# Performance work log

Measured on AMD Instinct MI355X. Metric: run time of the kernel, lower is better.

The kernel has to match this reference:

```python
import jax, jax.numpy as jnp
import numpy as np

N_LINKS = 10000
N_PATHS = 50000
PLEN = 5                 # fixed path length -> max_len
E = N_PATHS * PLEN       # number of (link, path) edge entries
D = 32                   # link_state_dim == path_state_dim
H = 32
RU = 256                 # readout_units
T_ITERS = 8              # message-passing iterations t


def setup_inputs() -> dict:
    key = jax.random.key(0)
    ks = jax.random.split(key, 20)
    s = 0.1
    inp = {}
    inp["traffic"] = jax.random.uniform(ks[0], (N_PATHS,), dtype=jnp.float32)
    inp["packets"] = jax.random.uniform(ks[1], (N_PATHS,), dtype=jnp.float32)
    inp["time_dist_params"] = jax.random.normal(ks[2], (N_PATHS, 12), dtype=jnp.float32)
    inp["capacity"] = jax.random.uniform(ks[3], (N_LINKS,), dtype=jnp.float32)
    # edge lists: each path has exactly PLEN links
    inp["link_to_path"] = jax.random.randint(ks[4], (E,), 0, N_LINKS, dtype=jnp.int32)
    inp["path_ids"] = jnp.repeat(jnp.arange(N_PATHS, dtype=jnp.int32), PLEN)
    inp["sequence_path"] = jnp.tile(jnp.arange(PLEN, dtype=jnp.int32), N_PATHS)
    inp["path_to_link"] = jax.random.randint(ks[5], (E,), 0, N_PATHS, dtype=jnp.int32)
    inp["sequence_links"] = jax.random.randint(ks[6], (E,), 0, N_LINKS, dtype=jnp.int32)
    inp["n_links"] = N_LINKS
    inp["n_paths"] = N_PATHS
    # path-update GRU (input D -> hidden H), torch layout [3H, in]
    inp["Wi_p"] = jax.random.normal(ks[7], (3 * H, D), dtype=jnp.float32) * s
    inp["Wh_p"] = jax.random.normal(ks[8], (3 * H, H), dtype=jnp.float32) * s
    inp["bi_p"] = jnp.zeros((3 * H,), jnp.float32)
    inp["bh_p"] = jnp.zeros((3 * H,), jnp.float32)
    # link-update GRUCell (input H -> hidden D)
    inp["Wi_l"] = jax.random.normal(ks[9], (3 * D, H), dtype=jnp.float32) * s
    inp["Wh_l"] = jax.random.normal(ks[10], (3 * D, D), dtype=jnp.float32) * s
    inp["bi_l"] = jnp.zeros((3 * D,), jnp.float32)
    inp["bh_l"] = jnp.zeros((3 * D,), jnp.float32)
    # readout MLP
    inp["W1"] = jax.random.normal(ks[11], (RU, H), dtype=jnp.float32) * s
    inp["b1"] = jnp.zeros((RU,), jnp.float32)
    inp["W2"] = jax.random.normal(ks[12], (RU, RU), dtype=jnp.float32) * s
    inp["b2"] = jnp.zeros((RU,), jnp.float32)
    inp["W3"] = jax.random.normal(ks[13], (1, RU), dtype=jnp.float32) * s
    inp["b3"] = jnp.zeros((1,), jnp.float32)
    return inp


def _gru_step(x, h, Wi, Wh, bi, bh):
    # torch GRU gate math
    gi = x @ Wi.T + bi
    gh = h @ Wh.T + bh
    ir, iz, in_ = jnp.split(gi, 3, axis=-1)
    hr, hz, hn = jnp.split(gh, 3, axis=-1)
    r = jax.nn.sigmoid(ir + hr)
    z = jax.nn.sigmoid(iz + hz)
    n = jnp.tanh(in_ + r * hn)
    return (1.0 - z) * n + z * h


def reference(traffic, packets, time_dist_params, capacity,
              link_to_path, path_ids, sequence_path, path_to_link, sequence_links,
              n_links, n_paths,
              Wi_p, Wh_p, bi_p, bh_p, Wi_l, Wh_l, bi_l, bh_l,
              W1, b1, W2, b2, W3, b3):
    max_len = PLEN  # == sequence_path.max() + 1 (static)
    # per-path valid lengths (equivalent to the torch nonzero-row count loop)
    lens = jax.ops.segment_max(sequence_path, path_ids, num_segments=n_paths) + 1
    link_state = jnp.concatenate(
        [capacity[:, None], jnp.zeros((n_links, D - 1), capacity.dtype)], axis=1)
    path_state = jnp.concatenate(
        [traffic[:, None], packets[:, None], time_dist_params,
         jnp.zeros((n_paths, D - 14), traffic.dtype)], axis=1)

    for _ in range(T_ITERS):
        link_gather = link_state[link_to_path]  # [E, D]
        link_inputs = jnp.zeros((n_paths, max_len, D), link_state.dtype)
        link_inputs = link_inputs.at[path_ids, sequence_path].set(link_gather)

        def step(h, xt_t):
            xt, t = xt_t
            h_new = _gru_step(xt, h, Wi_p, Wh_p, bi_p, bh_p)
            h = jnp.where((t < lens)[:, None], h_new, h)  # pack_padded semantics
            return h, None

        path_state, _ = jax.lax.scan(
            step, path_state,
            (jnp.swapaxes(link_inputs, 0, 1), jnp.arange(max_len)))

        path_gather = path_state[path_to_link]  # [E, H]
        path_sum = jnp.zeros((n_links, H), path_gather.dtype).at[sequence_links].add(path_gather)
        link_state = _gru_step(path_sum, link_state, Wi_l, Wh_l, bi_l, bh_l)

    r = jax.nn.relu(path_state @ W1.T + b1)
    r = jax.nn.relu(r @ W2.T + b2)
    r = r @ W3.T + b3            # [n_paths, 1]
    return r[:, 0][None, :]      # [1, n_paths]
```

## Files before the change

kernel.cpp:

```cpp
#include <hip/hip_runtime.h>

#define NP 50000
#define NL 10000
#define PLEN 5
#define NE (NP * PLEN)
#define DD 32
#define RUU 256
#define TITERS 8
#define PPW 8
#define LPW 2

__device__ __forceinline__ float sigmoidf_(float a) {
    return 1.0f / (1.0f + __expf(-a));
}
__device__ __forceinline__ float tanhf_(float a) {
    a = fminf(fmaxf(a, -15.0f), 15.0f);
    float t = __expf(2.0f * a);
    return (t - 1.0f) / (t + 1.0f);
}

__global__ __launch_bounds__(256) void k_init(
    const float* __restrict__ traffic, const float* __restrict__ packets,
    const float* __restrict__ tdp, const float* __restrict__ capacity,
    float* __restrict__ path_state, float* __restrict__ link_state,
    int* __restrict__ lens, int* __restrict__ cnt) {
    int i = blockIdx.x * 256 + threadIdx.x;
    if (i < NP) {
        float v[DD];
        v[0] = traffic[i];
        v[1] = packets[i];
#pragma unroll
        for (int k = 0; k < 12; k++) v[2 + k] = tdp[i * 12 + k];
#pragma unroll
        for (int k = 14; k < DD; k++) v[k] = 0.0f;
#pragma unroll
        for (int k = 0; k < DD; k++) path_state[i * DD + k] = v[k];
        lens[i] = 0;
    }
    if (i < NL) {
        link_state[i * DD] = capacity[i];
#pragma unroll
        for (int k = 1; k < DD; k++) link_state[i * DD + k] = 0.0f;
        cnt[i] = 0;
    }
}

__global__ __launch_bounds__(256) void k_lens(const int* __restrict__ path_ids,
                                              const int* __restrict__ seq_path,
                                              int* __restrict__ lens) {
    int e = blockIdx.x * 256 + threadIdx.x;
    if (e < NE) atomicMax(&lens[path_ids[e]], seq_path[e] + 1);
}

__global__ __launch_bounds__(256) void k_csr_count(const int* __restrict__ seq_links,
                                                   int* __restrict__ cnt) {
    int e = blockIdx.x * 256 + threadIdx.x;
    if (e < NE) atomicAdd(&cnt[seq_links[e]], 1);
}

__global__ __launch_bounds__(256) void k_csr_scan(const int* __restrict__ cnt,
                                                  int* __restrict__ offs,
                                                  int* __restrict__ cursor) {
    __shared__ int ssum[256];
    const int tid = threadIdx.x;
    const int CH = 40;
    int base = tid * CH;
    int s = 0;
    for (int i = 0; i < CH; i++) {
        int idx = base + i;
        s += (idx < NL) ? cnt[idx] : 0;
    }
    ssum[tid] = s;
    __syncthreads();
    for (int off = 1; off < 256; off <<= 1) {
        int t = (tid >= off) ? ssum[tid - off] : 0;
        __syncthreads();
        ssum[tid] += t;
        __syncthreads();
    }
    int run = ssum[tid] - s;
    for (int i = 0; i < CH; i++) {
        int idx = base + i;
        if (idx < NL) {
            offs[idx] = run;
            cursor[idx] = run;
            run += cnt[idx];
        }
    }
    if (tid == 0) offs[NL] = ssum[255];
}

__global__ __launch_bounds__(256) void k_csr_fill(const int* __restrict__ seq_links,
                                                  const int* __restrict__ path_to_link,
                                                  int* __restrict__ cursor,
                                                  int* __restrict__ csr_pids) {
    int e = blockIdx.x * 256 + threadIdx.x;
    if (e < NE) {
        int l = seq_links[e];
        int slot = atomicAdd(&cursor[l], 1);
        csr_pids[slot] = path_to_link[e];
    }
}

__global__ __launch_bounds__(256) void k_w2t(const float* __restrict__ W2,
                                             float* __restrict__ W2t) {
    int j = blockIdx.x, k = threadIdx.x;
    W2t[k * RUU + j] = W2[j * RUU + k];
}

__global__ __launch_bounds__(256, 2) void k_gru_paths(
    const float* __restrict__ link_state, float* __restrict__ path_state,
    const int* __restrict__ link_to_path, const int* __restrict__ lens,
    const float* __restrict__ Wi, const float* __restrict__ Wh,
    const float* __restrict__ bi, const float* __restrict__ bh) {
    const int tid = threadIdx.x;
    const int wave = tid >> 6;
    const int lane = tid & 63;
    const int d = lane & 31;
    const int half = lane >> 5;

    float wi[3][16], wh[3][16];
#pragma unroll
    for (int g = 0; g < 3; g++) {
        const float* wip = &Wi[(g * 32 + d) * 32 + half * 16];
        const float* whp = &Wh[(g * 32 + d) * 32 + half * 16];
#pragma unroll
        for (int c = 0; c < 4; c++) {
            *(float4*)&wi[g][c * 4] = *(const float4*)&wip[c * 4];
            *(float4*)&wh[g][c * 4] = *(const float4*)&whp[c * 4];
        }
    }
#pragma unroll
    for (int g = 0; g < 3; g++)
#pragma unroll
        for (int k = 0; k < 16; k++) {
            asm volatile("" : "+v"(wi[g][k]));
            asm volatile("" : "+v"(wh[g][k]));
        }
    const float bir = bi[d], biz = bi[d + 32], bin = bi[d + 64];
    const float bhr = bh[d], bhz = bh[d + 32], bhn = bh[d + 64];

    const int pbase = (blockIdx.x * 4 + wave) * PPW;
    for (int pp = 0; pp < PPW; pp++) {
        const int p = pbase + pp;
        if (p >= NP) break;

        float hd = path_state[p * DD + d];
        float hk[16];
#pragma unroll
        for (int c = 0; c < 4; c++)
            *(float4*)&hk[c * 4] = *(const float4*)&path_state[p * DD + half * 16 + c * 4];

        const int len = lens[p];
        int li[PLEN];
#pragma unroll
        for (int s = 0; s < PLEN; s++) li[s] = link_to_path[p * PLEN + s];

        float xk[16];
#pragma unroll
        for (int c = 0; c < 4; c++)
            *(float4*)&xk[c * 4] = *(const float4*)&link_state[li[0] * DD + half * 16 + c * 4];

#pragma unroll
        for (int st = 0; st < PLEN; st++) {
            float xn[16];
            if (st + 1 < PLEN) {
#pragma unroll
                for (int c = 0; c < 4; c++)
                    *(float4*)&xn[c * 4] =
                        *(const float4*)&link_state[li[st + 1] * DD + half * 16 + c * 4];
            }
            float ir = 0.f, iz = 0.f, in_ = 0.f, hr = 0.f, hz = 0.f, hn = 0.f;
#pragma unroll
            for (int k = 0; k < 16; k++) {
                ir  = fmaf(xk[k], wi[0][k], ir);
                iz  = fmaf(xk[k], wi[1][k], iz);
                in_ = fmaf(xk[k], wi[2][k], in_);
                hr  = fmaf(hk[k], wh[0][k], hr);
                hz  = fmaf(hk[k], wh[1][k], hz);
                hn  = fmaf(hk[k], wh[2][k], hn);
            }
            ir += __shfl_xor(ir, 32);
            iz += __shfl_xor(iz, 32);
            in_ += __shfl_xor(in_, 32);
            hr += __shfl_xor(hr, 32);
            hz += __shfl_xor(hz, 32);
            hn += __shfl_xor(hn, 32);
            float r = sigmoidf_(ir + bir + hr + bhr);
            float z = sigmoidf_(iz + biz + hz + bhz);
            float n = tanhf_(in_ + bin + r * (hn + bhn));
            float hnew = (1.0f - z) * n + z * hd;
            hd = (st < len) ? hnew : hd;
            int hdi = __float_as_int(hd);
#pragma unroll
            for (int k = 0; k < 16; k++) {
                int src = ((half << 4) + k) << 2;
                hk[k] = __int_as_float(__builtin_amdgcn_ds_bpermute(src, hdi));
            }
            if (st + 1 < PLEN) {
#pragma unroll
                for (int k = 0; k < 16; k++) xk[k] = xn[k];
            }
        }
        if (half == 0) path_state[p * DD + d] = hd;
    }
}

__global__ __launch_bounds__(256, 2) void k_links(
    const float* __restrict__ path_state, float* __restrict__ link_state,
    const int* __restrict__ offs, const int* __restrict__ csr_pids,
    const float* __restrict__ Wi, const float* __restrict__ Wh,
    const float* __restrict__ bi, const float* __restrict__ bh) {
    const int tid = threadIdx.x;
    const int wave = tid >> 6;
    const int lane = tid & 63;
    const int d = lane & 31;
    const int half = lane >> 5;

    float wi[3][16], wh[3][16];
#pragma unroll
    for (int g = 0; g < 3; g++) {
        const float* wip = &Wi[(g * 32 + d) * 32 + half * 16];
        const float* whp = &Wh[(g * 32 + d) * 32 + half * 16];
#pragma unroll
        for (int c = 0; c < 4; c++) {
            *(float4*)&wi[g][c * 4] = *(const float4*)&wip[c * 4];
            *(float4*)&wh[g][c * 4] = *(const float4*)&whp[c * 4];
        }
    }
#pragma unroll
    for (int g = 0; g < 3; g++)
#pragma unroll
        for (int k = 0; k < 16; k++) {
            asm volatile("" : "+v"(wi[g][k]));
            asm volatile("" : "+v"(wh[g][k]));
        }
    const float bir = bi[d], biz = bi[d + 32], bin = bi[d + 64];
    const float bhr = bh[d], bhz = bh[d + 32], bhn = bh[d + 64];

    const int lbase = (blockIdx.x * 4 + wave) * LPW;
    for (int ll = 0; ll < LPW; ll++) {
        const int l = lbase + ll;
        if (l >= NL) break;
        const int beg = offs[l], end = offs[l + 1];

        float xv = 0.f;
        int t = beg + half;
        int pid = (t < end) ? csr_pids[t] : 0;
        while (t < end) {
            int t2 = t + 2;
            int pid2 = (t2 < end) ? csr_pids[t2] : 0;
            xv += path_state[pid * DD + d];
            pid = pid2;
            t = t2;
        }
        xv += __shfl_xor(xv, 32);

        float hd = link_state[l * DD + d];
        float hk[16], xk[16];
#pragma unroll
        for (int c = 0; c < 4; c++)
            *(float4*)&hk[c * 4] = *(const float4*)&link_state[l * DD + half * 16 + c * 4];
        int xvi = __float_as_int(xv);
#pragma unroll
        for (int k = 0; k < 16; k++) {
            int src = ((half << 4) + k) << 2;
            xk[k] = __int_as_float(__builtin_amdgcn_ds_bpermute(src, xvi));
        }

        float ir = 0.f, iz = 0.f, in_ = 0.f, hr = 0.f, hz = 0.f, hn = 0.f;
#pragma unroll
        for (int k = 0; k < 16; k++) {
            ir  = fmaf(xk[k], wi[0][k], ir);
            iz  = fmaf(xk[k], wi[1][k], iz);
            in_ = fmaf(xk[k], wi[2][k], in_);
            hr  = fmaf(hk[k], wh[0][k], hr);
            hz  = fmaf(hk[k], wh[1][k], hz);
            hn  = fmaf(hk[k], wh[2][k], hn);
        }
        ir += __shfl_xor(ir, 32);
        iz += __shfl_xor(iz, 32);
        in_ += __shfl_xor(in_, 32);
        hr += __shfl_xor(hr, 32);
        hz += __shfl_xor(hz, 32);
        hn += __shfl_xor(hn, 32);
        float r = sigmoidf_(ir + bir + hr + bhr);
        float z = sigmoidf_(iz + biz + hz + bhz);
        float n = tanhf_(in_ + bin + r * (hn + bhn));
        float hnew = (1.0f - z) * n + z * hd;
        if (half == 0) link_state[l * DD + d] = hnew;
    }
}

__global__ __launch_bounds__(256, 2) void k_readout(
    const float* __restrict__ path_state, float* __restrict__ out,
    const float* __restrict__ W1, const float* __restrict__ b1,
    const float* __restrict__ W2t, const float* __restrict__ b2,
    const float* __restrict__ W3, const float* __restrict__ b3) {
    __shared__ float sr1[64 * RUU];
    const int tid = threadIdx.x;
    const int p0 = blockIdx.x * 64;

    float w1r[DD];
#pragma unroll
    for (int c = 0; c < 8; c++)
        *(float4*)&w1r[c * 4] = *(const float4*)&W1[tid * DD + c * 4];
    float bb1 = b1[tid];

#pragma unroll 2
    for (int m = 0; m < 64; m++) {
        int p = p0 + m;
        if (p >= NP) p = NP - 1;
        const float4* xr = (const float4*)&path_state[(size_t)p * DD];
        float acc = bb1;
#pragma unroll
        for (int c = 0; c < 8; c++) {
            float4 xv = xr[c];
            acc = fmaf(xv.x, w1r[c * 4 + 0], fmaf(xv.y, w1r[c * 4 + 1],
                  fmaf(xv.z, w1r[c * 4 + 2], fmaf(xv.w, w1r[c * 4 + 3], acc))));
        }
        sr1[m * RUU + tid] = fmaxf(acc, 0.0f);
    }
    __syncthreads();

    const int pig = tid >> 5;
    const int jg  = tid & 31;
    float accs[8][8];
#pragma unroll
    for (int jj = 0; jj < 8; jj++) {
        float bv = b2[jg * 8 + jj];
#pragma unroll
        for (int pp = 0; pp < 8; pp++) accs[pp][jj] = bv;
    }
    for (int k4 = 0; k4 < 64; k4++) {
        const int k0 = k4 * 4;
        float a[8][4];
#pragma unroll
        for (int pp = 0; pp < 8; pp++)
            *(float4*)&a[pp][0] = *(const float4*)&sr1[(pig * 8 + pp) * RUU + k0];
#pragma unroll
        for (int kk = 0; kk < 4; kk++) {
            float4 w0 = *(const float4*)&W2t[(size_t)(k0 + kk) * RUU + jg * 8];
            float4 w1_ = *(const float4*)&W2t[(size_t)(k0 + kk) * RUU + jg * 8 + 4];
#pragma unroll
            for (int pp = 0; pp < 8; pp++) {
                float av = a[pp][kk];
                accs[pp][0] = fmaf(av, w0.x, accs[pp][0]);
                accs[pp][1] = fmaf(av, w0.y, accs[pp][1]);
                accs[pp][2] = fmaf(av, w0.z, accs[pp][2]);
                accs[pp][3] = fmaf(av, w0.w, accs[pp][3]);
                accs[pp][4] = fmaf(av, w1_.x, accs[pp][4]);
                accs[pp][5] = fmaf(av, w1_.y, accs[pp][5]);
                accs[pp][6] = fmaf(av, w1_.z, accs[pp][6]);
                accs[pp][7] = fmaf(av, w1_.w, accs[pp][7]);
            }
        }
    }

    float w3r[8];
#pragma unroll
    for (int c = 0; c < 2; c++)
        *(float4*)&w3r[c * 4] = *(const float4*)&W3[jg * 8 + c * 4];
    float val[8];
#pragma unroll
    for (int pp = 0; pp < 8; pp++) {
        float v = 0.f;
#pragma unroll
        for (int jj = 0; jj < 8; jj++) v = fmaf(w3r[jj], fmaxf(accs[pp][jj], 0.f), v);
        val[pp] = v;
    }
#pragma unroll
    for (int m = 1; m < 32; m <<= 1)
#pragma unroll
        for (int pp = 0; pp < 8; pp++) val[pp] += __shfl_xor(val[pp], m);
    if (jg == 0) {
        float b3v = b3[0];
#pragma unroll
        for (int pp = 0; pp < 8; pp++) {
            int p = p0 + pig * 8 + pp;
            if (p < NP) out[p] = val[pp] + b3v;
        }
    }
}

extern "C" void kernel_launch(void* const* d_in, const int* in_sizes, int n_in,
                              void* d_out, int out_size, void* d_ws, size_t ws_size,
                              hipStream_t stream) {
    const float* traffic  = (const float*)d_in[0];
    const float* packets  = (const float*)d_in[1];
    const float* tdp      = (const float*)d_in[2];
    const float* capacity = (const float*)d_in[3];
    const int* link_to_path = (const int*)d_in[4];
    const int* path_ids     = (const int*)d_in[5];
    const int* seq_path     = (const int*)d_in[6];
    const int* path_to_link = (const int*)d_in[7];
    const int* seq_links    = (const int*)d_in[8];
    const float* Wi_p = (const float*)d_in[11];
    const float* Wh_p = (const float*)d_in[12];
    const float* bi_p = (const float*)d_in[13];
    const float* bh_p = (const float*)d_in[14];
    const float* Wi_l = (const float*)d_in[15];
    const float* Wh_l = (const float*)d_in[16];
    const float* bi_l = (const float*)d_in[17];
    const float* bh_l = (const float*)d_in[18];
    const float* W1 = (const float*)d_in[19];
    const float* b1 = (const float*)d_in[20];
    const float* W2 = (const float*)d_in[21];
    const float* b2 = (const float*)d_in[22];
    const float* W3 = (const float*)d_in[23];
    const float* b3 = (const float*)d_in[24];
    float* out = (float*)d_out;

    float* path_state = (float*)d_ws;
    float* link_state = path_state + (size_t)NP * DD;
    float* w2t        = link_state + (size_t)NL * DD;
    int* lens     = (int*)(w2t + RUU * RUU);
    int* cnt      = lens + NP;
    int* offs     = cnt + NL;
    int* cursor   = offs + NL + 1;
    int* csr_pids = cursor + NL;

    k_init<<<(NP + 255) / 256, 256, 0, stream>>>(traffic, packets, tdp, capacity,
                                                 path_state, link_state, lens, cnt);
    k_lens<<<(NE + 255) / 256, 256, 0, stream>>>(path_ids, seq_path, lens);
    k_csr_count<<<(NE + 255) / 256, 256, 0, stream>>>(seq_links, cnt);
    k_csr_scan<<<1, 256, 0, stream>>>(cnt, offs, cursor);
    k_csr_fill<<<(NE + 255) / 256, 256, 0, stream>>>(seq_links, path_to_link,
                                                     cursor, csr_pids);
    k_w2t<<<RUU, RUU, 0, stream>>>(W2, w2t);
    for (int t = 0; t < TITERS; t++) {
        k_gru_paths<<<(NP + 4 * PPW - 1) / (4 * PPW), 256, 0, stream>>>(
            link_state, path_state, link_to_path, lens, Wi_p, Wh_p, bi_p, bh_p);
        k_links<<<(NL + 4 * LPW - 1) / (4 * LPW), 256, 0, stream>>>(
            path_state, link_state, offs, csr_pids, Wi_l, Wh_l, bi_l, bh_l);
    }
    k_readout<<<(NP + 63) / 64, 256, 0, stream>>>(path_state, out, W1, b1, w2t,
                                                  b2, W3, b3);
}
```

Measured before the change: 1.477 ms.

## Split GRU input and hidden projections into phases to halve weight registers

Both GRU kernels now hold only one weight matrix in registers at a time. They first compute all input-gate projections for a block of paths or links into shared memory, then reload the registers with the hidden weights and run the recurrent step. The hidden-state broadcast moves from ds_bpermute to a small per-wave shared buffer. Launch bounds rise to four blocks per SIMD to raise occupancy and hide gather latency. The cost is extra LDS traffic and block-wide barriers, and the grid sizes now assume NP and NL divide evenly by 16.

Measured after the change: 1.371 ms. 7.2% less time.

```diff
diff --git a/kernel.cpp b/kernel.cpp
--- a/kernel.cpp
+++ b/kernel.cpp
@@ -7,8 +7,8 @@
 #define DD 32
 #define RUU 256
 #define TITERS 8
-#define PPW 8
-#define LPW 2
+#define PPB 16
+#define LPB 16
 
 __device__ __forceinline__ float sigmoidf_(float a) {
     return 1.0f / (1.0f + __expf(-a));
@@ -108,142 +108,128 @@
     W2t[k * RUU + j] = W2[j * RUU + k];
 }
 
-__global__ __launch_bounds__(256, 2) void k_gru_paths(
+__global__ __launch_bounds__(256, 4) void k_gru_paths(
     const float* __restrict__ link_state, float* __restrict__ path_state,
     const int* __restrict__ link_to_path, const int* __restrict__ lens,
     const float* __restrict__ Wi, const float* __restrict__ Wh,
     const float* __restrict__ bi, const float* __restrict__ bh) {
+    __shared__ float gi[PPB * PLEN * 96];
+    __shared__ float hbuf[4][DD];
     const int tid = threadIdx.x;
     const int wave = tid >> 6;
     const int lane = tid & 63;
     const int d = lane & 31;
     const int half = lane >> 5;
-
-    float wi[3][16], wh[3][16];
+    const int pl0 = wave * 4;
+    const int pbase = blockIdx.x * PPB;
+
+    float w[3][16];
 #pragma unroll
     for (int g = 0; g < 3; g++) {
-        const float* wip = &Wi[(g * 32 + d) * 32 + half * 16];
-        const float* whp = &Wh[(g * 32 + d) * 32 + half * 16];
-#pragma unroll
-        for (int c = 0; c < 4; c++) {
-            *(float4*)&wi[g][c * 4] = *(const float4*)&wip[c * 4];
-            *(float4*)&wh[g][c * 4] = *(const float4*)&whp[c * 4];
-        }
+        const float* wp = &Wi[(g * 32 + d) * 32 + half * 16];
+#pragma unroll
+        for (int c = 0; c < 4; c++) *(float4*)&w[g][c * 4] = *(const float4*)&wp[c * 4];
     }
 #pragma unroll
     for (int g = 0; g < 3; g++)
 #pragma unroll
-        for (int k = 0; k < 16; k++) {
-            asm volatile("" : "+v"(wi[g][k]));
-            asm volatile("" : "+v"(wh[g][k]));
-        }
-    const float bir = bi[d], biz = bi[d + 32], bin = bi[d + 64];
-    const float bhr = bh[d], bhz = bh[d + 32], bhn = bh[d + 64];
-
-    const int pbase = (blockIdx.x * 4 + wave) * PPW;
-    for (int pp = 0; pp < PPW; pp++) {
-        const int p = pbase + pp;
-        if (p >= NP) break;
-
+        for (int k = 0; k < 16; k++) asm volatile("" : "+v"(w[g][k]));
+    {
+        const float b0 = bi[d], b1_ = bi[d + 32], b2_ = bi[d + 64];
+        for (int j = 0; j < 4; j++) {
+            const int p = pbase + pl0 + j;
+#pragma unroll
+            for (int st = 0; st < PLEN; st++) {
+                const int li = link_to_path[p * PLEN + st];
+                float xk[16];
+#pragma unroll
+                for (int c = 0; c < 4; c++)
+                    *(float4*)&xk[c * 4] =
+                        *(const float4*)&link_state[li * DD + half * 16 + c * 4];
+                float s0 = 0.f, s1 = 0.f, s2 = 0.f;
+#pragma unroll
+                for (int k = 0; k < 16; k++) {
+                    s0 = fmaf(xk[k], w[0][k], s0);
+                    s1 = fmaf(xk[k], w[1][k], s1);
+                    s2 = fmaf(xk[k], w[2][k], s2);
+                }
+                s0 += __shfl_xor(s0, 32);
+                s1 += __shfl_xor(s1, 32);
+                s2 += __shfl_xor(s2, 32);
+                float* gp = &gi[((pl0 + j) * PLEN + st) * 96];
+                gp[d]      = s0 + b0;
+                gp[d + 32] = s1 + b1_;
+                gp[d + 64] = s2 + b2_;
+            }
+        }
+    }
+    __syncthreads();
+
+#pragma unroll
+    for (int g = 0; g < 3; g++) {
+        const float* wp = &Wh[(g * 32 + d) * 32 + half * 16];
+#pragma unroll
+        for (int c = 0; c < 4; c++) *(float4*)&w[g][c * 4] = *(const float4*)&wp[c * 4];
+    }
+#pragma unroll
+    for (int g = 0; g < 3; g++)
+#pragma unroll
+        for (int k = 0; k < 16; k++) asm volatile("" : "+v"(w[g][k]));
+    const float bh0 = bh[d], bh1 = bh[d + 32], bh2 = bh[d + 64];
+
+    for (int j = 0; j < 4; j++) {
+        const int p = pbase + pl0 + j;
+        const int len = lens[p];
         float hd = path_state[p * DD + d];
         float hk[16];
 #pragma unroll
         for (int c = 0; c < 4; c++)
             *(float4*)&hk[c * 4] = *(const float4*)&path_state[p * DD + half * 16 + c * 4];
-
-        const int len = lens[p];
-        int li[PLEN];
-#pragma unroll
-        for (int s = 0; s < PLEN; s++) li[s] = link_to_path[p * PLEN + s];
-
-        float xk[16];
-#pragma unroll
-        for (int c = 0; c < 4; c++)
-            *(float4*)&xk[c * 4] = *(const float4*)&link_state[li[0] * DD + half * 16 + c * 4];
-
 #pragma unroll
         for (int st = 0; st < PLEN; st++) {
-            float xn[16];
-            if (st + 1 < PLEN) {
-#pragma unroll
-                for (int c = 0; c < 4; c++)
-                    *(float4*)&xn[c * 4] =
-                        *(const float4*)&link_state[li[st + 1] * DD + half * 16 + c * 4];
+            float hr = 0.f, hz = 0.f, hn = 0.f;
+#pragma unroll
+            for (int k = 0; k < 16; k++) {
+                hr = fmaf(hk[k], w[0][k], hr);
+                hz = fmaf(hk[k], w[1][k], hz);
+                hn = fmaf(hk[k], w[2][k], hn);
             }
-            float ir = 0.f, iz = 0.f, in_ = 0.f, hr = 0.f, hz = 0.f, hn = 0.f;
-#pragma unroll
-            for (int k = 0; k < 16; k++) {
-                ir  = fmaf(xk[k], wi[0][k], ir);
-                iz  = fmaf(xk[k], wi[1][k], iz);
-                in_ = fmaf(xk[k], wi[2][k], in_);
-                hr  = fmaf(hk[k], wh[0][k], hr);
-                hz  = fmaf(hk[k], wh[1][k], hz);
-                hn  = fmaf(hk[k], wh[2][k], hn);
-            }
-            ir += __shfl_xor(ir, 32);
-            iz += __shfl_xor(iz, 32);
-            in_ += __shfl_xor(in_, 32);
             hr += __shfl_xor(hr, 32);
             hz += __shfl_xor(hz, 32);
             hn += __shfl_xor(hn, 32);
-            float r = sigmoidf_(ir + bir + hr + bhr);
-            float z = sigmoidf_(iz + biz + hz + bhz);
-            float n = tanhf_(in_ + bin + r * (hn + bhn));
+            const float* gp = &gi[((pl0 + j) * PLEN + st) * 96];
+            float gir = gp[d], giz = gp[d + 32], gin = gp[d + 64];
+            float r = sigmoidf_(gir + hr + bh0);
+            float z = sigmoidf_(giz + hz + bh1);
+            float n = tanhf_(gin + r * (hn + bh2));
             float hnew = (1.0f - z) * n + z * hd;
             hd = (st < len) ? hnew : hd;
-            int hdi = __float_as_int(hd);
-#pragma unroll
-            for (int k = 0; k < 16; k++) {
-                int src = ((half << 4) + k) << 2;
-                hk[k] = __int_as_float(__builtin_amdgcn_ds_bpermute(src, hdi));
-            }
-            if (st + 1 < PLEN) {
-#pragma unroll
-                for (int k = 0; k < 16; k++) xk[k] = xn[k];
-            }
+            hbuf[wave][d] = hd;
+#pragma unroll
+            for (int c = 0; c < 4; c++)
+                *(float4*)&hk[c * 4] = *(const float4*)&hbuf[wave][half * 16 + c * 4];
         }
         if (half == 0) path_state[p * DD + d] = hd;
     }
 }
 
-__global__ __launch_bounds__(256, 2) void k_links(
+__global__ __launch_bounds__(256, 4) void k_links(
     const float* __restrict__ path_state, float* __restrict__ link_state,
     const int* __restrict__ offs, const int* __restrict__ csr_pids,
     const float* __restrict__ Wi, const float* __restrict__ Wh,
     const float* __restrict__ bi, const float* __restrict__ bh) {
+    __shared__ float xsum[4][4][DD];
+    __shared__ float gil[4][4][96];
     const int tid = threadIdx.x;
     const int wave = tid >> 6;
     const int lane = tid & 63;
     const int d = lane & 31;
     const int half = lane >> 5;
-
-    float wi[3][16], wh[3][16];
-#pragma unroll
-    for (int g = 0; g < 3; g++) {
-        const float* wip = &Wi[(g * 32 + d) * 32 + half * 16];
-        const float* whp = &Wh[(g * 32 + d) * 32 + half * 16];
-#pragma unroll
-        for (int c = 0; c < 4; c++) {
-            *(float4*)&wi[g][c * 4] = *(const float4*)&wip[c * 4];
-            *(float4*)&wh[g][c * 4] = *(const float4*)&whp[c * 4];
-        }
-    }
-#pragma unroll
-    for (int g = 0; g < 3; g++)
-#pragma unroll
-        for (int k = 0; k < 16; k++) {
-            asm volatile("" : "+v"(wi[g][k]));
-            asm volatile("" : "+v"(wh[g][k]));
-        }
-    const float bir = bi[d], biz = bi[d + 32], bin = bi[d + 64];
-    const float bhr = bh[d], bhz = bh[d + 32], bhn = bh[d + 64];
-
-    const int lbase = (blockIdx.x * 4 + wave) * LPW;
-    for (int ll = 0; ll < LPW; ll++) {
-        const int l = lbase + ll;
-        if (l >= NL) break;
+    const int lbase = blockIdx.x * LPB + wave * 4;
+
+    for (int j = 0; j < 4; j++) {
+        const int l = lbase + j;
         const int beg = offs[l], end = offs[l + 1];
-
         float xv = 0.f;
         int t = beg + half;
         int pid = (t < end) ? csr_pids[t] : 0;
@@ -255,38 +241,77 @@
             t = t2;
         }
         xv += __shfl_xor(xv, 32);
-
+        xsum[wave][j][d] = xv;
+    }
+    __syncthreads();
+
+    float w[3][16];
+#pragma unroll
+    for (int g = 0; g < 3; g++) {
+        const float* wp = &Wi[(g * 32 + d) * 32 + half * 16];
+#pragma unroll
+        for (int c = 0; c < 4; c++) *(float4*)&w[g][c * 4] = *(const float4*)&wp[c * 4];
+    }
+#pragma unroll
+    for (int g = 0; g < 3; g++)
+#pragma unroll
+        for (int k = 0; k < 16; k++) asm volatile("" : "+v"(w[g][k]));
+    {
+        const float b0 = bi[d], b1_ = bi[d + 32], b2_ = bi[d + 64];
+        for (int j = 0; j < 4; j++) {
+            float xk[16];
+#pragma unroll
+            for (int c = 0; c < 4; c++)
+                *(float4*)&xk[c * 4] = *(const float4*)&xsum[wave][j][half * 16 + c * 4];
+            float s0 = 0.f, s1 = 0.f, s2 = 0.f;
+#pragma unroll
+            for (int k = 0; k < 16; k++) {
+                s0 = fmaf(xk[k], w[0][k], s0);
+                s1 = fmaf(xk[k], w[1][k], s1);
+                s2 = fmaf(xk[k], w[2][k], s2);
+            }
+            s0 += __shfl_xor(s0, 32);
+            s1 += __shfl_xor(s1, 32);
+            s2 += __shfl_xor(s2, 32);
+            gil[wave][j][d]      = s0 + b0;
+            gil[wave][j][d + 32] = s1 + b1_;
+            gil[wave][j][d + 64] = s2 + b2_;
+        }
+    }
+    __syncthreads();
+
+#pragma unroll
+    for (int g = 0; g < 3; g++) {
+        const float* wp = &Wh[(g * 32 + d) * 32 + half * 16];
+#pragma unroll
+        for (int c = 0; c < 4; c++) *(float4*)&w[g][c * 4] = *(const float4*)&wp[c * 4];
+    }
+#pragma unroll
+    for (int g = 0; g < 3; g++)
+#pragma unroll
+        for (int k = 0; k < 16; k++) asm volatile("" : "+v"(w[g][k]));
+    const float bh0 = bh[d], bh1 = bh[d + 32], bh2 = bh[d + 64];
+    for (int j = 0; j < 4; j++) {
+        const int l = lbase + j;
         float hd = link_state[l * DD + d];
-        float hk[16], xk[16];
+        float hk[16];
 #pragma unroll
         for (int c = 0; c < 4; c++)
             *(float4*)&hk[c * 4] = *(const float4*)&link_state[l * DD + half * 16 + c * 4];
-        int xvi = __float_as_int(xv);
+        float hr = 0.f, hz = 0.f, hn = 0.f;
 #pragma unroll
         for (int k = 0; k < 16; k++) {
-            int src = ((half << 4) + k) << 2;
-            xk[k] = __int_as_float(__builtin_amdgcn_ds_bpermute(src, xvi));
-        }
-
-        float ir = 0.f, iz = 0.f, in_ = 0.f, hr = 0.f, hz = 0.f, hn = 0.f;
-#pragma unroll
-        for (int k = 0; k < 16; k++) {
-            ir  = fmaf(xk[k], wi[0][k], ir);
-            iz  = fmaf(xk[k], wi[1][k], iz);
-            in_ = fmaf(xk[k], wi[2][k], in_);
-            hr  = fmaf(hk[k], wh[0][k], hr);
-            hz  = fmaf(hk[k], wh[1][k], hz);
-            hn  = fmaf(hk[k], wh[2][k], hn);
-        }
-        ir += __shfl_xor(ir, 32);
-        iz += __shfl_xor(iz, 32);
-        in_ += __shfl_xor(in_, 32);
+            hr = fmaf(hk[k], w[0][k], hr);
+            hz = fmaf(hk[k], w[1][k], hz);
+            hn = fmaf(hk[k], w[2][k], hn);
+        }
         hr += __shfl_xor(hr, 32);
         hz += __shfl_xor(hz, 32);
         hn += __shfl_xor(hn, 32);
-        float r = sigmoidf_(ir + bir + hr + bhr);
-        float z = sigmoidf_(iz + biz + hz + bhz);
-        float n = tanhf_(in_ + bin + r * (hn + bhn));
+        float gir = gil[wave][j][d], giz = gil[wave][j][d + 32], gin = gil[wave][j][d + 64];
+        float r = sigmoidf_(gir + hr + bh0);
+        float z = sigmoidf_(giz + hz + bh1);
+        float n = tanhf_(gin + r * (hn + bh2));
         float hnew = (1.0f - z) * n + z * hd;
         if (half == 0) link_state[l * DD + d] = hnew;
     }
@@ -429,11 +454,11 @@
                                                      cursor, csr_pids);
     k_w2t<<<RUU, RUU, 0, stream>>>(W2, w2t);
     for (int t = 0; t < TITERS; t++) {
-        k_gru_paths<<<(NP + 4 * PPW - 1) / (4 * PPW), 256, 0, stream>>>(
+        k_gru_paths<<<NP / PPB, 256, 0, stream>>>(
             link_state, path_state, link_to_path, lens, Wi_p, Wh_p, bi_p, bh_p);
-        k_links<<<(NL + 4 * LPW - 1) / (4 * LPW), 256, 0, stream>>>(
+        k_links<<<NL / LPB, 256, 0, stream>>>(
             path_state, link_state, offs, csr_pids, Wi_l, Wh_l, bi_l, bh_l);
     }
-    k_readout<<<(NP + 63) / 64, 256, 0, stream>>>(path_state, out, W1, b1, w2t,
-                                                  b2, W3, b3);
-}
+    k_readout<<<(NP + 63) / 64, 256, 0, stream>>>(path_state, out, W1, b1,
+                                                  w2t, b2, W3, b3);
+}
```
